# Optimization experiments

Hardware: AMD Instinct MI355X
Metric: run time of the kernel (lower is better)

## Reference

```python
import jax, jax.numpy as jnp
import numpy as np

IN_F = 256
OUT_F = 128
ALPHA = 0.2  # LeakyReLU negative slope
NEG_INF = -9.0e15


def setup_inputs() -> dict:
    key = jax.random.key(0)
    k_h, k_j, k_adj, k_w1, k_w2, k_a = jax.random.split(key, 6)
    B, N = 8, 2048
    h = jax.random.normal(k_h, (B, N, IN_F), dtype=jnp.float32)
    j = jax.random.normal(k_j, (B, N, IN_F), dtype=jnp.float32)
    adj = jax.random.randint(k_adj, (B, N, N), 0, 2, dtype=jnp.int32)
    # xavier_uniform with gain=1.414: bound = gain * sqrt(6/(fan_in+fan_out))
    def xavier(k, shape, gain=1.414):
        bound = gain * np.sqrt(6.0 / (shape[0] + shape[1]))
        return jax.random.uniform(k, shape, jnp.float32, -bound, bound)
    W1 = xavier(k_w1, (IN_F, OUT_F))
    W2 = xavier(k_w2, (IN_F, OUT_F))
    a = xavier(k_a, (2 * OUT_F, 1))
    return {"h": h, "j": j, "adj": adj, "W1": W1, "W2": W2, "a": a}


def reference(h, j, adj, W1, W2, a):
    # Projections: [B, N, OUT_F]
    Wh = jnp.einsum("bnf,fo->bno", h, W1)
    Wj = jnp.einsum("bnf,fo->bno", j, W2)
    # Additive attention logits: e[b,i,k] = leakyrelu(Wh@a1 [i] + Wh@a2 [k])
    Wh1 = Wh @ a[:OUT_F, :]   # [B, N, 1]
    Wh2 = Wh @ a[OUT_F:, :]   # [B, N, 1]
    e = jax.nn.leaky_relu(Wh1 + jnp.swapaxes(Wh2, 1, 2), negative_slope=ALPHA)
    # Mask non-edges, row-softmax over neighbors (dim=2)
    logits = jnp.where(adj > 0, e, NEG_INF)
    attention = jax.nn.softmax(logits, axis=2)
    # dropout skipped (eval mode). attention@Wh + attention@Wj == attention@(Wh+Wj)
    output = jnp.einsum("bik,bko->bio", attention, Wh + Wj)
    return jax.nn.elu(output)  # concat=True
```

## Files before the change

### kernel.cpp

```cpp
#include <hip/hip_runtime.h>
#include <hip/hip_bf16.h>

#define BATCH 8
#define NN 2048
#define IN_F 256
#define OUT_F 128
#define ALPHA 0.2f

typedef __attribute__((ext_vector_type(8))) short short8v;
typedef __attribute__((ext_vector_type(4))) float f32x4;

static __device__ __forceinline__ unsigned short f2bf(float x) {
    unsigned int u = __float_as_uint(x);
    u = (u + 0x7fffu + ((u >> 16) & 1u)) >> 16;
    return (unsigned short)u;
}

static __device__ __forceinline__ unsigned long long pk4(float a, float b, float c, float d) {
    union { unsigned long long ll; __hip_bfloat162 h2[2]; } u;
    u.h2[0] = __float22bfloat162_rn(make_float2(a, b));
    u.h2[1] = __float22bfloat162_rn(make_float2(c, d));
    return u.ll;
}

__global__ __launch_bounds__(256) void k_prew(
    const float* __restrict__ W1, const float* __restrict__ W2,
    const float* __restrict__ a,
    unsigned short* __restrict__ Wt, float* __restrict__ w1a1, float* __restrict__ w1a2)
{
    const int t = threadIdx.x;
    const int k8 = blockIdx.x * 8;
#pragma unroll
    for (int q = 0; q < 4; ++q) {
        const int idx = q * 256 + t;
        const int o = idx & 127;
        const int kk = k8 + (idx >> 7);
        const float v = (kk < IN_F) ? W1[kk * OUT_F + o] : W2[(kk - IN_F) * OUT_F + o];
        Wt[(size_t)o * 512 + kk] = f2bf(v);
    }
    if (k8 < IN_F) {
        const int lane = t & 63, w = t >> 6;
#pragma unroll
        for (int u = 0; u < 2; ++u) {
            const int kk = k8 + 2 * w + u;
            const float* wr = W1 + kk * OUT_F;
            float v1 = wr[lane] * a[lane] + wr[lane + 64] * a[lane + 64];
            float v2 = wr[lane] * a[OUT_F + lane] + wr[lane + 64] * a[OUT_F + lane + 64];
#pragma unroll
            for (int off = 32; off; off >>= 1) {
                v1 += __shfl_xor(v1, off);
                v2 += __shfl_xor(v2, off);
            }
            if (lane == 0) { w1a1[kk] = v1; w1a2[kk] = v2; }
        }
    }
}

#define BM 16

__global__ __launch_bounds__(256) void k_proj(
    const float* __restrict__ h, const float* __restrict__ j,
    const unsigned short* __restrict__ Wt,
    const float* __restrict__ w1a1g, const float* __restrict__ w1a2g,
    const int* __restrict__ adj,
    unsigned short* __restrict__ Vf, float* __restrict__ s1, float* __restrict__ s2,
    unsigned short* __restrict__ bits16)
{
    __shared__ __align__(16) unsigned short X[BM * 512];

    const int t = threadIdx.x, lane = t & 63, w = t >> 6;
    const int row0 = blockIdx.x * BM;
    const int b = row0 >> 11, n0 = row0 & 2047;

    const float4* wa1v = (const float4*)w1a1g;
    const float4* wa2v = (const float4*)w1a2g;

    const int srow = w * 4 + (lane >> 4);
    const int scol = lane & 15;
    const int sswz = (srow & 7) << 4;
    const float* hrow = h + (size_t)(row0 + srow) * IN_F;
    const float* jrow = j + (size_t)(row0 + srow) * IN_F;

    float d1 = 0.f, d2 = 0.f;
#pragma unroll
    for (int q = 0; q < 4; ++q) {
        const int f4 = q * 16 + scol;
        const float4 hv = ((const float4*)hrow)[f4];
        *(unsigned long long*)((char*)X + ((srow * 1024 + f4 * 8) ^ sswz)) =
            pk4(hv.x, hv.y, hv.z, hv.w);
        const float4 a1 = wa1v[f4], a2 = wa2v[f4];
        d1 += hv.x * a1.x + hv.y * a1.y + hv.z * a1.z + hv.w * a1.w;
        d2 += hv.x * a2.x + hv.y * a2.y + hv.z * a2.z + hv.w * a2.w;
    }
#pragma unroll
    for (int q = 0; q < 4; ++q) {
        const int f4 = q * 16 + scol;
        const float4 jv = ((const float4*)jrow)[f4];
        *(unsigned long long*)((char*)X + ((srow * 1024 + 512 + f4 * 8) ^ sswz)) =
            pk4(jv.x, jv.y, jv.z, jv.w);
    }
    d1 += __shfl_xor(d1, 1); d1 += __shfl_xor(d1, 2);
    d1 += __shfl_xor(d1, 4); d1 += __shfl_xor(d1, 8);
    d2 += __shfl_xor(d2, 1); d2 += __shfl_xor(d2, 2);
    d2 += __shfl_xor(d2, 4); d2 += __shfl_xor(d2, 8);
    if (scol == 0) { s1[row0 + srow] = d1; s2[row0 + srow] = d2; }
    __syncthreads();

    const unsigned short* wb = Wt + (size_t)(w * 32 + (lane & 15)) * 512 + ((lane >> 4) * 8);
    const int abase = (lane & 15) * 1024 + ((lane >> 4) * 16);
    const int aswz = (lane & 7) << 4;

    f32x4 acc0 = {0.f, 0.f, 0.f, 0.f}, acc1 = {0.f, 0.f, 0.f, 0.f};
#pragma unroll
    for (int ks = 0; ks < 16; ++ks) {
        const short8v af = *(const short8v*)((const char*)X + ((abase + ks * 64) ^ aswz));
        const short8v b0 = *(const short8v*)(wb + ks * 32);
        const short8v b1 = *(const short8v*)(wb + 16 * 512 + ks * 32);
        acc0 = __builtin_amdgcn_mfma_f32_16x16x32_bf16(af, b0, acc0, 0, 0, 0);
        acc1 = __builtin_amdgcn_mfma_f32_16x16x32_bf16(af, b1, acc1, 0, 0, 0);
    }

    const int nn = n0 + (lane >> 4) * 4;
    const size_t vbase = (size_t)b * 524288
                       + ((size_t)(nn >> 5) << 13)
                       + (((nn & 31) >> 3) << 4) + ((nn & 7) << 1);
#pragma unroll
    for (int f = 0; f < 2; ++f) {
        const f32x4 ac = f ? acc1 : acc0;
        const int o = w * 32 + f * 16 + (lane & 15);
        *(unsigned long long*)((char*)Vf + vbase + o * 64) = pk4(ac[0], ac[1], ac[2], ac[3]);
    }

    const int gstride = 1024 * 256;
    for (int g = blockIdx.x * 256 + t; g < (BATCH * NN * NN) / 16; g += gstride) {
        const int4* ap = (const int4*)(adj + (size_t)g * 16);
        const int4 x0 = ap[0], x1 = ap[1], x2 = ap[2], x3 = ap[3];
        unsigned m = 0;
        m |= (x0.x > 0) ? 1u : 0u;        m |= (x0.y > 0) ? 2u : 0u;
        m |= (x0.z > 0) ? 4u : 0u;        m |= (x0.w > 0) ? 8u : 0u;
        m |= (x1.x > 0) ? 16u : 0u;       m |= (x1.y > 0) ? 32u : 0u;
        m |= (x1.z > 0) ? 64u : 0u;       m |= (x1.w > 0) ? 128u : 0u;
        m |= (x2.x > 0) ? 256u : 0u;      m |= (x2.y > 0) ? 512u : 0u;
        m |= (x2.z > 0) ? 1024u : 0u;     m |= (x2.w > 0) ? 2048u : 0u;
        m |= (x3.x > 0) ? 4096u : 0u;     m |= (x3.y > 0) ? 8192u : 0u;
        m |= (x3.z > 0) ? 16384u : 0u;    m |= (x3.w > 0) ? 32768u : 0u;
        bits16[g] = (unsigned short)m;
    }
}

#define IBLK 32

__global__ __launch_bounds__(256, 3) void k_attn(
    const unsigned char* __restrict__ bits, const unsigned short* __restrict__ Vf,
    const float* __restrict__ s1g, const float* __restrict__ s2g,
    float* __restrict__ out)
{
    __shared__ __align__(16) char smem[33792];
    __shared__ float rs_lds[4][IBLK];
    __shared__ float wmaxs[4];
    __shared__ __align__(16) float lut[16][4];

    float* e2_lds = (float*)smem;
    float* f2_lds = (float*)(smem + 8192);
    unsigned int* bitw = (unsigned int*)(smem + 16384);
    float* comb = (float*)smem;

    const int t = threadIdx.x, lane = t & 63, w = t >> 6;
    const int orig = blockIdx.x;
    const int b = orig & 7;
    const int r = orig >> 3;
    const int oh = r >> 6;
    const int i0 = (r & 63) << 5;

    if (t < 16) {
        lut[t][0] = (float)(t & 1);
        lut[t][1] = (float)((t >> 1) & 1);
        lut[t][2] = (float)((t >> 2) & 1);
        lut[t][3] = (float)((t >> 3) & 1);
    }

    {
        const unsigned int* bg = (const unsigned int*)(bits + ((size_t)b * NN + i0) * 256);
#pragma unroll
        for (int q = 0; q < 8; ++q) {
            const int idx = q * 256 + t;
            bitw[(idx >> 6) * 65 + (idx & 63)] = bg[idx];
        }
    }

    const float4* s2v = (const float4*)(s2g + b * NN);
    float lmax = -1e30f;
#pragma unroll
    for (int q = 0; q < 2; ++q) {
        const int idx = q * 256 + t;
        const float4 v = s2v[idx];
        ((float4*)e2_lds)[idx] = make_float4(__expf(v.x), __expf(v.y),
                                             __expf(v.z), __expf(v.w));
        ((float4*)f2_lds)[idx] = make_float4(__expf(ALPHA * v.x), __expf(ALPHA * v.y),
                                             __expf(ALPHA * v.z), __expf(ALPHA * v.w));
        lmax = fmaxf(fmaxf(lmax, fmaxf(v.x, v.y)), fmaxf(v.z, v.w));
    }
#pragma unroll
    for (int off = 32; off; off >>= 1) lmax = fmaxf(lmax, __shfl_xor(lmax, off));
    if (lane == 0) wmaxs[w] = lmax;

    const int irow = lane & 15;
    const int kcb = lane >> 4;
    const int kw = w * 512;

    const float s1r0 = s1g[b * NN + i0 + irow];
    const float s1r1 = s1g[b * NN + i0 + 16 + irow];
    __syncthreads();
    const float s2max = fmaxf(fmaxf(wmaxs[0], wmaxs[1]), fmaxf(wmaxs[2], wmaxs[3]));
    const float mx0 = s1r0 + s2max, mx1 = s1r1 + s2max;
    const float mA0 = fmaxf(mx0, ALPHA * mx0);
    const float mA1 = fmaxf(mx1, ALPHA * mx1);
    const float c0 = __expf(s1r0 - mA0), d0 = __expf(ALPHA * s1r0 - mA0);
    const float c1 = __expf(s1r1 - mA1), d1 = __expf(ALPHA * s1r1 - mA1);

    const float* e2p = e2_lds + kw + kcb * 8;
    const float* f2p = f2_lds + kw + kcb * 8;
    const char* vfb = (const char*)Vf + (size_t)b * 524288 + (size_t)(w * 16) * 8192
                    + (size_t)(oh * 64 + irow) * 64 + (size_t)kcb * 16;
    const unsigned int* bw0p = bitw + irow * 65 + w * 16;
    const unsigned int* bw1p = bitw + (16 + irow) * 65 + w * 16;

    short8v vone;
#pragma unroll
    for (int q = 0; q < 8; ++q) vone[q] = (short)0x3F80;

    f32x4 acc0[4], acc1[4];
    f32x4 acc_ps0 = {0.f, 0.f, 0.f, 0.f}, acc_ps1 = {0.f, 0.f, 0.f, 0.f};
#pragma unroll
    for (int og = 0; og < 4; ++og) {
        acc0[og] = (f32x4){0.f, 0.f, 0.f, 0.f};
        acc1[og] = (f32x4){0.f, 0.f, 0.f, 0.f};
    }

#pragma unroll
    for (int ks = 0; ks < 16; ++ks) {
        const char* vk = vfb + (size_t)ks * 8192;
        const short8v vf0 = *(const short8v*)(vk);
        const short8v vf1 = *(const short8v*)(vk + 1024);
        const short8v vf2 = *(const short8v*)(vk + 2048);
        const short8v vf3 = *(const short8v*)(vk + 3072);

        const unsigned int bb0 = (bw0p[ks] >> (kcb * 8)) & 0xffu;
        const unsigned int bb1 = (bw1p[ks] >> (kcb * 8)) & 0xffu;
        const float4 m00 = ((const float4*)lut)[bb0 & 15], m01 = ((const float4*)lut)[bb0 >> 4];
        const float4 m10 = ((const float4*)lut)[bb1 & 15], m11 = ((const float4*)lut)[bb1 >> 4];

        const float4 ea = *(const float4*)(e2p + ks * 32);
        const float4 eb = *(const float4*)(e2p + ks * 32 + 4);
        const float4 fa = *(const float4*)(f2p + ks * 32);
        const float4 fb = *(const float4*)(f2p + ks * 32 + 4);
        const float e2r[8] = {ea.x, ea.y, ea.z, ea.w, eb.x, eb.y, eb.z, eb.w};
        const float f2r[8] = {fa.x, fa.y, fa.z, fa.w, fb.x, fb.y, fb.z, fb.w};
        const float mk0[8] = {m00.x, m00.y, m00.z, m00.w, m01.x, m01.y, m01.z, m01.w};
        const float mk1[8] = {m10.x, m10.y, m10.z, m10.w, m11.x, m11.y, m11.z, m11.w};

        float p0[8], p1[8];
#pragma unroll
        for (int e = 0; e < 8; ++e) {
            p0[e] = fmaxf(c0 * e2r[e], d0 * f2r[e]) * mk0[e];
            p1[e] = fmaxf(c1 * e2r[e], d1 * f2r[e]) * mk1[e];
        }
        union { short8v v; __hip_bfloat162 h2[4]; } pb0, pb1;
#pragma unroll
        for (int q = 0; q < 4; ++q) {
            pb0.h2[q] = __float22bfloat162_rn(make_float2(p0[2 * q], p0[2 * q + 1]));
            pb1.h2[q] = __float22bfloat162_rn(make_float2(p1[2 * q], p1[2 * q + 1]));
        }

        acc_ps0 = __builtin_amdgcn_mfma_f32_16x16x32_bf16(vone, pb0.v, acc_ps0, 0, 0, 0);
        acc_ps1 = __builtin_amdgcn_mfma_f32_16x16x32_bf16(vone, pb1.v, acc_ps1, 0, 0, 0);
        acc0[0] = __builtin_amdgcn_mfma_f32_16x16x32_bf16(vf0, pb0.v, acc0[0], 0, 0, 0);
        acc1[0] = __builtin_amdgcn_mfma_f32_16x16x32_bf16(vf0, pb1.v, acc1[0], 0, 0, 0);
        acc0[1] = __builtin_amdgcn_mfma_f32_16x16x32_bf16(vf1, pb0.v, acc0[1], 0, 0, 0);
        acc1[1] = __builtin_amdgcn_mfma_f32_16x16x32_bf16(vf1, pb1.v, acc1[1], 0, 0, 0);
        acc0[2] = __builtin_amdgcn_mfma_f32_16x16x32_bf16(vf2, pb0.v, acc0[2], 0, 0, 0);
        acc1[2] = __builtin_amdgcn_mfma_f32_16x16x32_bf16(vf2, pb1.v, acc1[2], 0, 0, 0);
        acc0[3] = __builtin_amdgcn_mfma_f32_16x16x32_bf16(vf3, pb0.v, acc0[3], 0, 0, 0);
        acc1[3] = __builtin_amdgcn_mfma_f32_16x16x32_bf16(vf3, pb1.v, acc1[3], 0, 0, 0);
    }

    if (lane < 16) {
        rs_lds[w][lane] = acc_ps0[0];
        rs_lds[w][16 + lane] = acc_ps1[0];
    }

    __syncthreads();
#pragma unroll
    for (int og = 0; og < 4; ++og) {
#pragma unroll
        for (int rr = 0; rr < 4; ++rr) {
            const int ol = og * 16 + kcb * 4 + rr;
            comb[(w * 64 + ol) * 33 + irow] = acc0[og][rr];
            comb[(w * 64 + ol) * 33 + 16 + irow] = acc1[og][rr];
        }
    }
    __syncthreads();

    const int i = t >> 3, oc = t & 7;
    const float tot = rs_lds[0][i] + rs_lds[1][i] + rs_lds[2][i] + rs_lds[3][i];
    const float inv = 1.0f / tot;
    float res[8];
#pragma unroll
    for (int u = 0; u < 8; ++u) {
        const int ol = oc * 8 + u;
        float v = comb[ol * 33 + i] + comb[(64 + ol) * 33 + i]
                + comb[(128 + ol) * 33 + i] + comb[(192 + ol) * 33 + i];
        v *= inv;
        res[u] = (v > 0.f) ? v : expm1f(v);
    }
    float4* ob = (float4*)(out + ((size_t)b * NN + i0 + i) * OUT_F + oh * 64 + oc * 8);
    ob[0] = make_float4(res[0], res[1], res[2], res[3]);
    ob[1] = make_float4(res[4], res[5], res[6], res[7]);
}

extern "C" void kernel_launch(void* const* d_in, const int* in_sizes, int n_in,
                              void* d_out, int out_size, void* d_ws, size_t ws_size,
                              hipStream_t stream) {
    const float* h  = (const float*)d_in[0];
    const float* j  = (const float*)d_in[1];
    const int* adj  = (const int*)d_in[2];
    const float* W1 = (const float*)d_in[3];
    const float* W2 = (const float*)d_in[4];
    const float* a  = (const float*)d_in[5];
    float* out = (float*)d_out;

    char* ws = (char*)d_ws;
    unsigned short* Vf = (unsigned short*)ws;
    ws += (size_t)BATCH * OUT_F * NN * 2;
    float* s1 = (float*)ws; ws += (size_t)BATCH * NN * 4;
    float* s2 = (float*)ws; ws += (size_t)BATCH * NN * 4;
    unsigned short* Wt = (unsigned short*)ws; ws += 128 * 512 * 2;
    float* w1a1 = (float*)ws; ws += 512 * 4;
    float* w1a2 = (float*)ws; ws += 512 * 4;
    unsigned char* bits = (unsigned char*)ws;

    k_prew<<<64, 256, 0, stream>>>(W1, W2, a, Wt, w1a1, w1a2);
    k_proj<<<(BATCH * NN) / BM, 256, 0, stream>>>(h, j, Wt, w1a1, w1a2, adj,
                                                  Vf, s1, s2, (unsigned short*)bits);
    k_attn<<<(BATCH * NN) / IBLK * 2, 256, 0, stream>>>(bits, Vf, s1, s2, out);
}
```

Baseline: 63.13 us.

## Compute all output features per attention block instead of splitting halves

```diff
diff --git a/kernel.cpp b/kernel.cpp
--- a/kernel.cpp
+++ b/kernel.cpp
@@ -150,12 +150,12 @@
 
 #define IBLK 32
 
-__global__ __launch_bounds__(256, 3) void k_attn(
+__global__ __launch_bounds__(256, 2) void k_attn(
     const unsigned char* __restrict__ bits, const unsigned short* __restrict__ Vf,
     const float* __restrict__ s1g, const float* __restrict__ s2g,
     float* __restrict__ out)
 {
-    __shared__ __align__(16) char smem[33792];
+    __shared__ __align__(16) char smem[34816];
     __shared__ float rs_lds[4][IBLK];
     __shared__ float wmaxs[4];
     __shared__ __align__(16) float lut[16][4];
@@ -168,9 +168,7 @@
     const int t = threadIdx.x, lane = t & 63, w = t >> 6;
     const int orig = blockIdx.x;
     const int b = orig & 7;
-    const int r = orig >> 3;
-    const int oh = r >> 6;
-    const int i0 = (r & 63) << 5;
+    const int i0 = (orig >> 3) << 5;
 
     if (t < 16) {
         lut[t][0] = (float)(t & 1);
@@ -221,7 +219,7 @@
     const float* e2p = e2_lds + kw + kcb * 8;
     const float* f2p = f2_lds + kw + kcb * 8;
     const char* vfb = (const char*)Vf + (size_t)b * 524288 + (size_t)(w * 16) * 8192
-                    + (size_t)(oh * 64 + irow) * 64 + (size_t)kcb * 16;
+                    + (size_t)irow * 64 + (size_t)kcb * 16;
     const unsigned int* bw0p = bitw + irow * 65 + w * 16;
     const unsigned int* bw1p = bitw + (16 + irow) * 65 + w * 16;
 
@@ -229,10 +227,10 @@
 #pragma unroll
     for (int q = 0; q < 8; ++q) vone[q] = (short)0x3F80;
 
-    f32x4 acc0[4], acc1[4];
-    f32x4 acc_ps0 = {0.f, 0.f, 0.f, 0.f}, acc_ps1 = {0.f, 0.f, 0.f, 0.f};
-#pragma unroll
-    for (int og = 0; og < 4; ++og) {
+    f32x4 acc0[8], acc1[8];
+    f32x4 ps0 = {0.f, 0.f, 0.f, 0.f}, ps1 = {0.f, 0.f, 0.f, 0.f};
+#pragma unroll
+    for (int og = 0; og < 8; ++og) {
         acc0[og] = (f32x4){0.f, 0.f, 0.f, 0.f};
         acc1[og] = (f32x4){0.f, 0.f, 0.f, 0.f};
     }
@@ -240,10 +238,10 @@
 #pragma unroll
     for (int ks = 0; ks < 16; ++ks) {
         const char* vk = vfb + (size_t)ks * 8192;
-        const short8v vf0 = *(const short8v*)(vk);
-        const short8v vf1 = *(const short8v*)(vk + 1024);
-        const short8v vf2 = *(const short8v*)(vk + 2048);
-        const short8v vf3 = *(const short8v*)(vk + 3072);
+        short8v vf[8];
+#pragma unroll
+        for (int og = 0; og < 8; ++og)
+            vf[og] = *(const short8v*)(vk + og * 1024);
 
         const unsigned int bb0 = (bw0p[ks] >> (kcb * 8)) & 0xffu;
         const unsigned int bb1 = (bw1p[ks] >> (kcb * 8)) & 0xffu;
@@ -272,50 +270,71 @@
             pb1.h2[q] = __float22bfloat162_rn(make_float2(p1[2 * q], p1[2 * q + 1]));
         }
 
-        acc_ps0 = __builtin_amdgcn_mfma_f32_16x16x32_bf16(vone, pb0.v, acc_ps0, 0, 0, 0);
-        acc_ps1 = __builtin_amdgcn_mfma_f32_16x16x32_bf16(vone, pb1.v, acc_ps1, 0, 0, 0);
-        acc0[0] = __builtin_amdgcn_mfma_f32_16x16x32_bf16(vf0, pb0.v, acc0[0], 0, 0, 0);
-        acc1[0] = __builtin_amdgcn_mfma_f32_16x16x32_bf16(vf0, pb1.v, acc1[0], 0, 0, 0);
-        acc0[1] = __builtin_amdgcn_mfma_f32_16x16x32_bf16(vf1, pb0.v, acc0[1], 0, 0, 0);
-        acc1[1] = __builtin_amdgcn_mfma_f32_16x16x32_bf16(vf1, pb1.v, acc1[1], 0, 0, 0);
-        acc0[2] = __builtin_amdgcn_mfma_f32_16x16x32_bf16(vf2, pb0.v, acc0[2], 0, 0, 0);
-        acc1[2] = __builtin_amdgcn_mfma_f32_16x16x32_bf16(vf2, pb1.v, acc1[2], 0, 0, 0);
-        acc0[3] = __builtin_amdgcn_mfma_f32_16x16x32_bf16(vf3, pb0.v, acc0[3], 0, 0, 0);
-        acc1[3] = __builtin_amdgcn_mfma_f32_16x16x32_bf16(vf3, pb1.v, acc1[3], 0, 0, 0);
+        ps0 = __builtin_amdgcn_mfma_f32_16x16x32_bf16(vone, pb0.v, ps0, 0, 0, 0);
+        ps1 = __builtin_amdgcn_mfma_f32_16x16x32_bf16(vone, pb1.v, ps1, 0, 0, 0);
+#pragma unroll
+        for (int og = 0; og < 8; ++og) {
+            acc0[og] = __builtin_amdgcn_mfma_f32_16x16x32_bf16(vf[og], pb0.v, acc0[og], 0, 0, 0);
+            acc1[og] = __builtin_amdgcn_mfma_f32_16x16x32_bf16(vf[og], pb1.v, acc1[og], 0, 0, 0);
+        }
     }
 
     if (lane < 16) {
-        rs_lds[w][lane] = acc_ps0[0];
-        rs_lds[w][16 + lane] = acc_ps1[0];
-    }
-
-    __syncthreads();
-#pragma unroll
-    for (int og = 0; og < 4; ++og) {
-#pragma unroll
-        for (int rr = 0; rr < 4; ++rr) {
-            const int ol = og * 16 + kcb * 4 + rr;
-            comb[(w * 64 + ol) * 33 + irow] = acc0[og][rr];
-            comb[(w * 64 + ol) * 33 + 16 + irow] = acc1[og][rr];
-        }
-    }
-    __syncthreads();
-
-    const int i = t >> 3, oc = t & 7;
-    const float tot = rs_lds[0][i] + rs_lds[1][i] + rs_lds[2][i] + rs_lds[3][i];
-    const float inv = 1.0f / tot;
-    float res[8];
-#pragma unroll
-    for (int u = 0; u < 8; ++u) {
-        const int ol = oc * 8 + u;
-        float v = comb[ol * 33 + i] + comb[(64 + ol) * 33 + i]
-                + comb[(128 + ol) * 33 + i] + comb[(192 + ol) * 33 + i];
-        v *= inv;
-        res[u] = (v > 0.f) ? v : expm1f(v);
-    }
-    float4* ob = (float4*)(out + ((size_t)b * NN + i0 + i) * OUT_F + oh * 64 + oc * 8);
-    ob[0] = make_float4(res[0], res[1], res[2], res[3]);
-    ob[1] = make_float4(res[4], res[5], res[6], res[7]);
+        rs_lds[w][lane] = ps0[0];
+        rs_lds[w][16 + lane] = ps1[0];
+    }
+
+    __syncthreads();
+
+#pragma unroll
+    for (int og = 0; og < 8; ++og)
+#pragma unroll
+        for (int rr = 0; rr < 4; ++rr)
+            comb[(w * 128 + og * 16 + kcb * 4 + rr) * 17 + irow] = acc0[og][rr];
+    __syncthreads();
+    {
+        const int i = t >> 4, oc = t & 15;
+        const float tot = rs_lds[0][i] + rs_lds[1][i] + rs_lds[2][i] + rs_lds[3][i];
+        const float inv = 1.0f / tot;
+        float res[8];
+#pragma unroll
+        for (int u = 0; u < 8; ++u) {
+            const int ol = oc * 8 + u;
+            float v = comb[ol * 17 + i] + comb[(128 + ol) * 17 + i]
+                    + comb[(256 + ol) * 17 + i] + comb[(384 + ol) * 17 + i];
+            v *= inv;
+            res[u] = (v > 0.f) ? v : expm1f(v);
+        }
+        float4* ob = (float4*)(out + ((size_t)b * NN + i0 + i) * OUT_F + oc * 8);
+        ob[0] = make_float4(res[0], res[1], res[2], res[3]);
+        ob[1] = make_float4(res[4], res[5], res[6], res[7]);
+    }
+    __syncthreads();
+
+#pragma unroll
+    for (int og = 0; og < 8; ++og)
+#pragma unroll
+        for (int rr = 0; rr < 4; ++rr)
+            comb[(w * 128 + og * 16 + kcb * 4 + rr) * 17 + irow] = acc1[og][rr];
+    __syncthreads();
+    {
+        const int i = t >> 4, oc = t & 15;
+        const float tot = rs_lds[0][16 + i] + rs_lds[1][16 + i]
+                        + rs_lds[2][16 + i] + rs_lds[3][16 + i];
+        const float inv = 1.0f / tot;
+        float res[8];
+#pragma unroll
+        for (int u = 0; u < 8; ++u) {
+            const int ol = oc * 8 + u;
+            float v = comb[ol * 17 + i] + comb[(128 + ol) * 17 + i]
+                    + comb[(256 + ol) * 17 + i] + comb[(384 + ol) * 17 + i];
+            v *= inv;
+            res[u] = (v > 0.f) ? v : expm1f(v);
+        }
+        float4* ob = (float4*)(out + ((size_t)b * NN + i0 + 16 + i) * OUT_F + oc * 8);
+        ob[0] = make_float4(res[0], res[1], res[2], res[3]);
+        ob[1] = make_float4(res[4], res[5], res[6], res[7]);
+    }
 }
 
 extern "C" void kernel_launch(void* const* d_in, const int* in_sizes, int n_in,
@@ -342,5 +361,5 @@
     k_prew<<<64, 256, 0, stream>>>(W1, W2, a, Wt, w1a1, w1a2);
     k_proj<<<(BATCH * NN) / BM, 256, 0, stream>>>(h, j, Wt, w1a1, w1a2, adj,
                                                   Vf, s1, s2, (unsigned short*)bits);
-    k_attn<<<(BATCH * NN) / IBLK * 2, 256, 0, stream>>>(bits, Vf, s1, s2, out);
-}
+    k_attn<<<(BATCH * NN) / IBLK, 256, 0, stream>>>(bits, Vf, s1, s2, out);
+}
```

Result: slower. 71.65 us (+13.5%).
